# Performance work log

Measured on AMD Instinct MI355X. Metric: run time of the kernel, lower is better.

Reference implementation:

```python
import jax, jax.numpy as jnp
import numpy as np

N_GO, N_KE, D = 8000, 2000, 16
N_LAYERS, N_TISSUE, DRUG = 3, 512, 2048
B = 256


def _scatter_add(msgs, dst, n):
    # msgs: [B, E, D] -> [B, n, D], summing messages into destination nodes
    Bm, _, d = msgs.shape
    return jnp.zeros((Bm, n, d), msgs.dtype).at[:, dst, :].add(msgs)


def setup_inputs() -> dict:
    key = jax.random.key(0)
    ks = jax.random.split(key, 20)
    inp = {
        "x": jax.random.normal(ks[0], (B, N_GO + DRUG), jnp.float32),
        "go_ke_src": jax.random.randint(ks[1], (50000,), 0, N_GO),
        "go_ke_dst": jax.random.randint(ks[2], (50000,), 0, N_KE),
        "ke_ke_src": jax.random.randint(ks[3], (20000,), 0, N_KE),
        "ke_ke_dst": jax.random.randint(ks[4], (20000,), 0, N_KE),
        "tissue": jax.random.randint(ks[5], (N_TISSUE,), 0, N_KE),
    }
    def w(k, shape, fan_in):
        return jax.random.normal(k, shape, jnp.float32) / np.sqrt(fan_in)
    inp["W_dec"] = w(ks[6], (N_GO, D), 1.0)          # per-GO scalar->vector layer
    inp["b_dec"] = jnp.zeros((N_GO, D), jnp.float32)
    inp["W_g2k"] = w(ks[7], (D, D), D)
    inp["b_g2k"] = jnp.zeros((D,), jnp.float32)
    inp["W_kk"] = w(ks[8], (N_LAYERS, D, D), D)
    inp["b_kk"] = jnp.zeros((N_LAYERS, D), jnp.float32)
    inp["w_ke"] = w(ks[9], (D,), D)                   # node readout D->1
    inp["b_ke"] = jnp.zeros((), jnp.float32)
    inp["W_bio1"] = w(ks[10], (N_TISSUE, 256), N_TISSUE)
    inp["b_bio1"] = jnp.zeros((256,), jnp.float32)
    inp["W_bio2"] = w(ks[11], (256, 128), 256)
    inp["b_bio2"] = jnp.zeros((128,), jnp.float32)
    inp["W_drug1"] = w(ks[12], (DRUG, 512), DRUG)
    inp["b_drug1"] = jnp.zeros((512,), jnp.float32)
    inp["W_drug2"] = w(ks[13], (512, 128), 512)
    inp["b_drug2"] = jnp.zeros((128,), jnp.float32)
    inp["W_pred"] = w(ks[14], (256, 1), 256)
    inp["b_pred"] = jnp.zeros((1,), jnp.float32)
    return inp


def reference(x, go_ke_src, go_ke_dst, ke_ke_src, ke_ke_dst, tissue,
              W_dec, b_dec, W_g2k, b_g2k, W_kk, b_kk, w_ke, b_ke,
              W_bio1, b_bio1, W_bio2, b_bio2,
              W_drug1, b_drug1, W_drug2, b_drug2, W_pred, b_pred):
    # go_decode_layer: per-GO scalar -> D-dim node feature
    go = jnp.tanh(x[:, :-DRUG, None] * W_dec + b_dec)          # [B, N_GO, D]
    # go2ke: gather source GO features, scatter-add into KE nodes, transform
    ke = _scatter_add(go[:, go_ke_src, :], go_ke_dst, N_KE)    # [B, N_KE, D]
    ke = jnp.tanh(ke @ W_g2k + b_g2k)
    # ke2ke message-passing layers
    for l in range(W_kk.shape[0]):
        agg = _scatter_add(ke[:, ke_ke_src, :], ke_ke_dst, N_KE)
        ke = jnp.tanh((ke + agg) @ W_kk[l] + b_kk[l])
    # ke_layer: per-node readout D -> scalar
    ke = jnp.tanh(jnp.einsum('bnd,d->bn', ke, w_ke) + b_ke)    # [B, N_KE]
    # tissue gather + bio MLP head
    bio = ke[:, tissue]                                         # [B, N_TISSUE]
    bio = jax.nn.relu(bio @ W_bio1 + b_bio1)
    bio = jax.nn.relu(bio @ W_bio2 + b_bio2)
    # drug fingerprint MLP head
    drug = x[:, -DRUG:]
    drug = jax.nn.relu(drug @ W_drug1 + b_drug1)
    drug = jax.nn.relu(drug @ W_drug2 + b_drug2)
    # predictor on concatenated features
    comb = jnp.concatenate([bio, drug], axis=-1)                # [B, 256]
    return comb @ W_pred + b_pred                               # [B, 1]
```

## Files before the change

### kernel.cpp

```cpp
#include <hip/hip_runtime.h>
#include <hip/hip_bf16.h>
#include <cstdint>
#include <cstddef>

#define BATCH 256
#define NGO   8000
#define NKE   2000
#define DD    16
#define XCOLS 10048
#define NDRUG 2048
#define NT    512
#define NSLAB 8
#define SB    32

__device__ __forceinline__ float tanh_fast(float z) {
    float e = __builtin_amdgcn_exp2f(z * 2.885390081777926f);
    float r = __builtin_amdgcn_rcpf(e + 1.0f);
    return fmaf(-2.0f, r, 1.0f);
}

__device__ __forceinline__ void add4(float4& a, const float4 b) {
    a.x += b.x; a.y += b.y; a.z += b.z; a.w += b.w;
}

__global__ void k_hist2(const int* __restrict__ gd, const int* __restrict__ kd,
                        int* __restrict__ cg, int* __restrict__ ck, int Eg, int Ek) {
    int e = blockIdx.x * 256 + threadIdx.x;
    if (e < Eg) atomicAdd(&cg[gd[e]], 1);
    else if (e < Eg + Ek) atomicAdd(&ck[kd[e - Eg]], 1);
}

__global__ void k_scan2(const int* __restrict__ cnt_go, const int* __restrict__ cnt_kk,
                        int* __restrict__ rp_go, int* __restrict__ rp_kk) {
    const int* cnt = blockIdx.x ? cnt_kk : cnt_go;
    int* rowptr    = blockIdx.x ? rp_kk  : rp_go;
    __shared__ int s[2048];
    int t = threadIdx.x;
    s[t]        = (t        < NKE) ? cnt[t]        : 0;
    s[t + 1024] = (t + 1024 < NKE) ? cnt[t + 1024] : 0;
    __syncthreads();
    for (int st = 1; st < 2048; st <<= 1) {
        int v0 = (t >= st) ? s[t - st] : 0;
        int v1 = s[t + 1024 - st];
        __syncthreads();
        s[t] += v0; s[t + 1024] += v1;
        __syncthreads();
    }
    if (t == 0) rowptr[0] = 0;
    rowptr[t + 1] = s[t];
    if (t + 1024 < NKE) rowptr[t + 1025] = s[t + 1024];
}

__global__ void k_fill2(const int* __restrict__ gs, const int* __restrict__ gdst,
                        const int* __restrict__ ks, const int* __restrict__ kdst,
                        int Eg, int Ek,
                        const int* __restrict__ rp_go, int* __restrict__ cur_go, int* __restrict__ col_go,
                        const int* __restrict__ rp_kk, int* __restrict__ cur_kk, int* __restrict__ col_kk) {
    int e = blockIdx.x * 256 + threadIdx.x;
    if (e < Eg) {
        int d = gdst[e];
        int p = atomicAdd(&cur_go[d], 1);
        col_go[rp_go[d] + p] = gs[e];
    } else if (e < Eg + Ek) {
        int e2 = e - Eg;
        int d = kdst[e2];
        int p = atomicAdd(&cur_kk[d], 1);
        col_kk[rp_kk[d] + p] = ks[e2];
    }
}

__global__ __launch_bounds__(256) void k_txpose(const float* __restrict__ x, float* __restrict__ xT) {
    __shared__ float tile[64][69];
    int c4 = threadIdx.x & 15, rr = threadIdx.x >> 4;
    int n0 = blockIdx.x * 64, b0 = blockIdx.y * 64;
#pragma unroll
    for (int i = 0; i < 4; i++) {
        int row = rr + i * 16;
        float4 v = *(const float4*)&x[(size_t)(b0 + row) * XCOLS + n0 + c4 * 4];
        tile[row][c4 * 4 + 0] = v.x; tile[row][c4 * 4 + 1] = v.y;
        tile[row][c4 * 4 + 2] = v.z; tile[row][c4 * 4 + 3] = v.w;
    }
    __syncthreads();
#pragma unroll
    for (int i = 0; i < 4; i++) {
        int nrow = rr + i * 16;
        float4 w;
        w.x = tile[c4 * 4 + 0][nrow]; w.y = tile[c4 * 4 + 1][nrow];
        w.z = tile[c4 * 4 + 2][nrow]; w.w = tile[c4 * 4 + 3][nrow];
        *(float4*)&xT[(size_t)(n0 + nrow) * 256 + b0 + c4 * 4] = w;
    }
}

__global__ __launch_bounds__(128) void k_fuse(const float* __restrict__ xT,
                                              const int* __restrict__ rowptr,
                                              const int* __restrict__ col,
                                              const float* __restrict__ Wd,
                                              const float* __restrict__ bd,
                                              const float* __restrict__ W,
                                              const float* __restrict__ bias,
                                              float* __restrict__ ke) {
    __shared__ float pre[32 * 17];
    __shared__ float Ws[256];
    __shared__ float bs[16];
    int s = blockIdx.x & 7, n = blockIdx.x >> 3;
    int tid = threadIdx.x;
    Ws[tid] = W[tid]; Ws[tid + 128] = W[tid + 128];
    if (tid < 16) bs[tid] = bias[tid];
    int bloc = tid >> 2, d4 = tid & 3;
    int bglob = s * SB + bloc;
    const float4* Wd4 = (const float4*)Wd;
    const float4* bd4 = (const float4*)bd;

    float4 acc = make_float4(0, 0, 0, 0);
    int e = rowptr[n], end = rowptr[n + 1];
    for (; e + 1 < end; e += 2) {
        int s0 = col[e], s1 = col[e + 1];
        float  xv0 = xT[(size_t)s0 * 256 + bglob];
        float  xv1 = xT[(size_t)s1 * 256 + bglob];
        float4 w0 = Wd4[s0 * 4 + d4], w1 = Wd4[s1 * 4 + d4];
        float4 c0 = bd4[s0 * 4 + d4], c1 = bd4[s1 * 4 + d4];
        acc.x += tanh_fast(fmaf(xv0, w0.x, c0.x)) + tanh_fast(fmaf(xv1, w1.x, c1.x));
        acc.y += tanh_fast(fmaf(xv0, w0.y, c0.y)) + tanh_fast(fmaf(xv1, w1.y, c1.y));
        acc.z += tanh_fast(fmaf(xv0, w0.z, c0.z)) + tanh_fast(fmaf(xv1, w1.z, c1.z));
        acc.w += tanh_fast(fmaf(xv0, w0.w, c0.w)) + tanh_fast(fmaf(xv1, w1.w, c1.w));
    }
    if (e < end) {
        int s0 = col[e];
        float  xv0 = xT[(size_t)s0 * 256 + bglob];
        float4 w0 = Wd4[s0 * 4 + d4];
        float4 c0 = bd4[s0 * 4 + d4];
        acc.x += tanh_fast(fmaf(xv0, w0.x, c0.x));
        acc.y += tanh_fast(fmaf(xv0, w0.y, c0.y));
        acc.z += tanh_fast(fmaf(xv0, w0.z, c0.z));
        acc.w += tanh_fast(fmaf(xv0, w0.w, c0.w));
    }
    pre[bloc * 17 + d4 * 4 + 0] = acc.x;
    pre[bloc * 17 + d4 * 4 + 1] = acc.y;
    pre[bloc * 17 + d4 * 4 + 2] = acc.z;
    pre[bloc * 17 + d4 * 4 + 3] = acc.w;
    __syncthreads();

    float4 o;
    float* op = &o.x;
#pragma unroll
    for (int q = 0; q < 4; q++) {
        int dp = d4 * 4 + q;
        float a = bs[dp];
#pragma unroll
        for (int d = 0; d < 16; d++) a = fmaf(pre[bloc * 17 + d], Ws[d * 16 + dp], a);
        op[q] = tanh_fast(a);
    }
    *(float4*)&ke[((size_t)s * NKE + n) * 512 + bloc * 16 + d4 * 4] = o;
}

__global__ __launch_bounds__(128) void k_layer(const float* __restrict__ kin,
                                               const int* __restrict__ rowptr,
                                               const int* __restrict__ col,
                                               const float* __restrict__ W,
                                               const float* __restrict__ bias,
                                               float* __restrict__ kout) {
    __shared__ float pre[32 * 17];
    __shared__ float Ws[256];
    __shared__ float bs[16];
    int s = blockIdx.x & 7, n = blockIdx.x >> 3;
    int tid = threadIdx.x;
    Ws[tid] = W[tid]; Ws[tid + 128] = W[tid + 128];
    if (tid < 16) bs[tid] = bias[tid];
    int bloc = tid >> 2, d4 = tid & 3;
    size_t slab_base = (size_t)s * NKE * 512;

    float4 acc = *(const float4*)&kin[slab_base + (size_t)n * 512 + tid * 4];
    int e = rowptr[n], end = rowptr[n + 1];
    for (; e + 1 < end; e += 2) {
        float4 v0 = *(const float4*)&kin[slab_base + (size_t)col[e]     * 512 + tid * 4];
        float4 v1 = *(const float4*)&kin[slab_base + (size_t)col[e + 1] * 512 + tid * 4];
        add4(acc, v0); add4(acc, v1);
    }
    if (e < end) {
        float4 v0 = *(const float4*)&kin[slab_base + (size_t)col[e] * 512 + tid * 4];
        add4(acc, v0);
    }
    pre[bloc * 17 + d4 * 4 + 0] = acc.x;
    pre[bloc * 17 + d4 * 4 + 1] = acc.y;
    pre[bloc * 17 + d4 * 4 + 2] = acc.z;
    pre[bloc * 17 + d4 * 4 + 3] = acc.w;
    __syncthreads();

    float4 o;
    float* op = &o.x;
#pragma unroll
    for (int q = 0; q < 4; q++) {
        int dp = d4 * 4 + q;
        float a = bs[dp];
#pragma unroll
        for (int d = 0; d < 16; d++) a = fmaf(pre[bloc * 17 + d], Ws[d * 16 + dp], a);
        op[q] = tanh_fast(a);
    }
    *(float4*)&kout[slab_base + (size_t)n * 512 + bloc * 16 + d4 * 4] = o;
}

__global__ __launch_bounds__(256) void k_kescalar(const float* __restrict__ ke,
                                                  const int* __restrict__ tissue,
                                                  const float* __restrict__ wke,
                                                  const float* __restrict__ bke,
                                                  float* __restrict__ bioT) {
    int t = blockIdx.x, b = threadIdx.x;
    int n = tissue[t];
    int s = b >> 5, bloc = b & 31;
    const float4* kp = (const float4*)&ke[((size_t)s * NKE + n) * 512 + bloc * 16];
    const float4* wp = (const float4*)wke;
    float4 k0 = kp[0], k1 = kp[1], k2 = kp[2], k3 = kp[3];
    float4 w0 = wp[0], w1 = wp[1], w2 = wp[2], w3 = wp[3];
    float acc = bke[0];
    acc += k0.x * w0.x + k0.y * w0.y + k0.z * w0.z + k0.w * w0.w;
    acc += k1.x * w1.x + k1.y * w1.y + k1.z * w1.z + k1.w * w1.w;
    acc += k2.x * w2.x + k2.y * w2.y + k2.z * w2.z + k2.w * w2.w;
    acc += k3.x * w3.x + k3.y * w3.y + k3.z * w3.z + k3.w * w3.w;
    bioT[t * 256 + b] = tanh_fast(acc);
}

__global__ __launch_bounds__(256) void k_txd(const float* __restrict__ x, float* __restrict__ xdT) {
    int t = blockIdx.x, b = threadIdx.x;
    xdT[t * 256 + b] = x[(size_t)b * XCOLS + NGO + t];
}

__global__ __launch_bounds__(256) void k_gemm(const float* __restrict__ A,
                                              const float* __restrict__ W,
                                              float* __restrict__ Cpart,
                                              int N, int Kper) {
    __shared__ float As[32][68];
    __shared__ float Ws[32][68];
    int tid = threadIdx.x;
    int tx = tid & 15, ty = tid >> 4;
    int jt = blockIdx.x * 64, bt = blockIdx.y * 64;
    int ks = blockIdx.z;
    int k0 = ks * Kper;

    float acc[4][4];
#pragma unroll
    for (int i = 0; i < 4; i++)
#pragma unroll
        for (int j = 0; j < 4; j++) acc[i][j] = 0.0f;

    for (int kc = 0; kc < Kper; kc += 32) {
#pragma unroll
        for (int i = 0; i < 8; i++) {
            int idx = tid + i * 256;
            int kk = idx >> 6, cc = idx & 63;
            As[kk][cc] = A[(size_t)(k0 + kc + kk) * 256 + bt + cc];
            Ws[kk][cc] = W[(size_t)(k0 + kc + kk) * N + jt + cc];
        }
        __syncthreads();
#pragma unroll 8
        for (int kk = 0; kk < 32; kk++) {
            float4 a = *(const float4*)&As[kk][tx * 4];
            float4 w = *(const float4*)&Ws[kk][ty * 4];
            acc[0][0] = fmaf(w.x, a.x, acc[0][0]); acc[0][1] = fmaf(w.x, a.y, acc[0][1]);
            acc[0][2] = fmaf(w.x, a.z, acc[0][2]); acc[0][3] = fmaf(w.x, a.w, acc[0][3]);
            acc[1][0] = fmaf(w.y, a.x, acc[1][0]); acc[1][1] = fmaf(w.y, a.y, acc[1][1]);
            acc[1][2] = fmaf(w.y, a.z, acc[1][2]); acc[1][3] = fmaf(w.y, a.w, acc[1][3]);
            acc[2][0] = fmaf(w.z, a.x, acc[2][0]); acc[2][1] = fmaf(w.z, a.y, acc[2][1]);
            acc[2][2] = fmaf(w.z, a.z, acc[2][2]); acc[2][3] = fmaf(w.z, a.w, acc[2][3]);
            acc[3][0] = fmaf(w.w, a.x, acc[3][0]); acc[3][1] = fmaf(w.w, a.y, acc[3][1]);
            acc[3][2] = fmaf(w.w, a.z, acc[3][2]); acc[3][3] = fmaf(w.w, a.w, acc[3][3]);
        }
        __syncthreads();
    }
#pragma unroll
    for (int jy = 0; jy < 4; jy++) {
        int j = jt + ty * 4 + jy;
        float4 v = make_float4(acc[jy][0], acc[jy][1], acc[jy][2], acc[jy][3]);
        *(float4*)&Cpart[((size_t)ks * N + j) * 256 + bt + tx * 4] = v;
    }
}

__global__ __launch_bounds__(256) void k_red(const float* __restrict__ Cpart,
                                             const float* __restrict__ bias,
                                             float* __restrict__ C, int N, int S) {
    int j = blockIdx.x, b = threadIdx.x;
    float acc = bias[j];
    for (int s = 0; s < S; s++) acc += Cpart[((size_t)s * N + j) * 256 + b];
    C[j * 256 + b] = fmaxf(acc, 0.0f);
}

__global__ __launch_bounds__(256) void k_final(const float* __restrict__ bio2T,
                                               const float* __restrict__ drug2T,
                                               const float* __restrict__ Wp,
                                               const float* __restrict__ bp,
                                               float* __restrict__ out) {
    int b = threadIdx.x;
    float acc = bp[0];
#pragma unroll 8
    for (int i = 0; i < 128; i++) acc = fmaf(bio2T[i * 256 + b], Wp[i], acc);
#pragma unroll 8
    for (int i = 0; i < 128; i++) acc = fmaf(drug2T[i * 256 + b], Wp[128 + i], acc);
    out[b] = acc;
}

extern "C" void kernel_launch(void* const* d_in, const int* in_sizes, int n_in,
                              void* d_out, int out_size, void* d_ws, size_t ws_size,
                              hipStream_t stream) {
    const float* x       = (const float*)d_in[0];
    const int*   go_src  = (const int*)d_in[1];
    const int*   go_dst  = (const int*)d_in[2];
    const int*   kk_src  = (const int*)d_in[3];
    const int*   kk_dst  = (const int*)d_in[4];
    const int*   tissue  = (const int*)d_in[5];
    const float* W_dec   = (const float*)d_in[6];
    const float* b_dec   = (const float*)d_in[7];
    const float* W_g2k   = (const float*)d_in[8];
    const float* b_g2k   = (const float*)d_in[9];
    const float* W_kk    = (const float*)d_in[10];
    const float* b_kk    = (const float*)d_in[11];
    const float* w_ke    = (const float*)d_in[12];
    const float* b_ke    = (const float*)d_in[13];
    const float* W_bio1  = (const float*)d_in[14];
    const float* b_bio1  = (const float*)d_in[15];
    const float* W_bio2  = (const float*)d_in[16];
    const float* b_bio2  = (const float*)d_in[17];
    const float* W_drug1 = (const float*)d_in[18];
    const float* b_drug1 = (const float*)d_in[19];
    const float* W_drug2 = (const float*)d_in[20];
    const float* b_drug2 = (const float*)d_in[21];
    const float* W_pred  = (const float*)d_in[22];
    const float* b_pred  = (const float*)d_in[23];
    float* out = (float*)d_out;

    const int E_GO = in_sizes[1];
    const int E_KK = in_sizes[3];

    char* wsb = (char*)d_ws;
    size_t off = 0;
    float* xT      = (float*)(wsb + off); off += (size_t)NGO * 256 * 4;
    float* ke_a    = (float*)(wsb + off); off += (size_t)NSLAB * NKE * 512 * 4;
    float* ke_b    = (float*)(wsb + off); off += (size_t)NSLAB * NKE * 512 * 4;
    float* bio_inT = (float*)(wsb + off); off += (size_t)NT * 256 * 4;
    float* bio1T   = (float*)(wsb + off); off += (size_t)256 * 256 * 4;
    float* bio2T   = (float*)(wsb + off); off += (size_t)128 * 256 * 4;
    float* xdT     = (float*)(wsb + off); off += (size_t)NDRUG * 256 * 4;
    float* drug1T  = (float*)(wsb + off); off += (size_t)512 * 256 * 4;
    float* drug2T  = (float*)(wsb + off); off += (size_t)128 * 256 * 4;
    float* cpart   = (float*)(wsb + off); off += (size_t)8 * 512 * 256 * 4;
    int* cnt_go    = (int*)(wsb + off); off += 2048 * 4;
    int* cur_go    = (int*)(wsb + off); off += 2048 * 4;
    int* cnt_kk    = (int*)(wsb + off); off += 2048 * 4;
    int* cur_kk    = (int*)(wsb + off); off += 2048 * 4;
    int* rp_go     = (int*)(wsb + off); off += 2048 * 4;
    int* rp_kk     = (int*)(wsb + off); off += 2048 * 4;
    int* col_go    = (int*)(wsb + off); off += 50048 * 4;
    int* col_kk    = (int*)(wsb + off); off += 20048 * 4;

    hipMemsetAsync(cnt_go, 0, 4 * 2048 * 4, stream);

    int Etot = E_GO + E_KK;
    k_hist2<<<(Etot + 255) / 256, 256, 0, stream>>>(go_dst, kk_dst, cnt_go, cnt_kk, E_GO, E_KK);
    k_scan2<<<2, 1024, 0, stream>>>(cnt_go, cnt_kk, rp_go, rp_kk);
    k_fill2<<<(Etot + 255) / 256, 256, 0, stream>>>(go_src, go_dst, kk_src, kk_dst, E_GO, E_KK,
                                                    rp_go, cur_go, col_go, rp_kk, cur_kk, col_kk);

    k_txpose<<<dim3(NGO / 64, 4), 256, 0, stream>>>(x, xT);
    k_fuse<<<NKE * NSLAB, 128, 0, stream>>>(xT, rp_go, col_go, W_dec, b_dec, W_g2k, b_g2k, ke_a);
    k_layer<<<NKE * NSLAB, 128, 0, stream>>>(ke_a, rp_kk, col_kk, W_kk + 0 * 256, b_kk + 0 * 16, ke_b);
    k_layer<<<NKE * NSLAB, 128, 0, stream>>>(ke_b, rp_kk, col_kk, W_kk + 1 * 256, b_kk + 1 * 16, ke_a);
    k_layer<<<NKE * NSLAB, 128, 0, stream>>>(ke_a, rp_kk, col_kk, W_kk + 2 * 256, b_kk + 2 * 16, ke_b);
    k_kescalar<<<NT, 256, 0, stream>>>(ke_b, tissue, w_ke, b_ke, bio_inT);

    k_txd<<<NDRUG, 256, 0, stream>>>(x, xdT);
    k_gemm<<<dim3(512 / 64, 4, 8), 256, 0, stream>>>(xdT, W_drug1, cpart, 512, 2048 / 8);
    k_red<<<512, 256, 0, stream>>>(cpart, b_drug1, drug1T, 512, 8);
    k_gemm<<<dim3(128 / 64, 4, 4), 256, 0, stream>>>(drug1T, W_drug2, cpart, 128, 512 / 4);
    k_red<<<128, 256, 0, stream>>>(cpart, b_drug2, drug2T, 128, 4);

    k_gemm<<<dim3(256 / 64, 4, 4), 256, 0, stream>>>(bio_inT, W_bio1, cpart, 256, 512 / 4);
    k_red<<<256, 256, 0, stream>>>(cpart, b_bio1, bio1T, 256, 4);
    k_gemm<<<dim3(128 / 64, 4, 2), 256, 0, stream>>>(bio1T, W_bio2, cpart, 128, 256 / 2);
    k_red<<<128, 256, 0, stream>>>(cpart, b_bio2, bio2T, 128, 2);

    k_final<<<1, 256, 0, stream>>>(bio2T, drug2T, W_pred, b_pred, out);
}
```

Measured before the change: 244.2 us.

## Fuse split-K reductions into consumers, merge transposes, prescale tanh inputs

Merges the GO transpose, drug transpose and a bias prescale into one prep kernel. The split-K reduce kernels are removed: each consumer GEMM or the final kernel now sums the partials and applies bias and ReLU while loading. In the fused gather kernel the inputs and biases are prescaled by the tanh constant, and the -2 and +1 tanh terms are hoisted out of the edge loop using the node degree. The k_layer gather loop is unrolled from 2 to 4 loads. Together these cut launch count and per-edge arithmetic, at the cost of redundant partial-sum reads inside the GEMM tile loads.

```diff
diff --git a/kernel.cpp b/kernel.cpp
--- a/kernel.cpp
+++ b/kernel.cpp
@@ -12,11 +12,17 @@
 #define NT    512
 #define NSLAB 8
 #define SB    32
+#define TANH_SCALE 2.885390081777926f
 
 __device__ __forceinline__ float tanh_fast(float z) {
-    float e = __builtin_amdgcn_exp2f(z * 2.885390081777926f);
+    float e = __builtin_amdgcn_exp2f(z * TANH_SCALE);
     float r = __builtin_amdgcn_rcpf(e + 1.0f);
     return fmaf(-2.0f, r, 1.0f);
+}
+
+__device__ __forceinline__ float rcp_core(float zp) {
+    float e = __builtin_amdgcn_exp2f(zp);
+    return __builtin_amdgcn_rcpf(e + 1.0f);
 }
 
 __device__ __forceinline__ void add4(float4& a, const float4 b) {
@@ -69,10 +75,23 @@
     }
 }
 
-__global__ __launch_bounds__(256) void k_txpose(const float* __restrict__ x, float* __restrict__ xT) {
+__global__ __launch_bounds__(256) void k_prep(const float* __restrict__ x,
+                                              float* __restrict__ xT,
+                                              float* __restrict__ xdT,
+                                              const float* __restrict__ bd,
+                                              float* __restrict__ bds) {
+    int bid = blockIdx.x;
+    if (bid >= 628) {
+        int i = (bid - 628) * 256 + threadIdx.x;
+        bds[i] = bd[i] * TANH_SCALE;
+        return;
+    }
     __shared__ float tile[64][69];
     int c4 = threadIdx.x & 15, rr = threadIdx.x >> 4;
-    int n0 = blockIdx.x * 64, b0 = blockIdx.y * 64;
+    int n0, b0;
+    bool isgo = bid < 500;
+    if (isgo) { n0 = (bid % 125) * 64; b0 = (bid / 125) * 64; }
+    else      { int t = bid - 500; n0 = NGO + (t & 31) * 64; b0 = (t >> 5) * 64; }
 #pragma unroll
     for (int i = 0; i < 4; i++) {
         int row = rr + i * 16;
@@ -87,7 +106,12 @@
         float4 w;
         w.x = tile[c4 * 4 + 0][nrow]; w.y = tile[c4 * 4 + 1][nrow];
         w.z = tile[c4 * 4 + 2][nrow]; w.w = tile[c4 * 4 + 3][nrow];
-        *(float4*)&xT[(size_t)(n0 + nrow) * 256 + b0 + c4 * 4] = w;
+        if (isgo) {
+            w.x *= TANH_SCALE; w.y *= TANH_SCALE; w.z *= TANH_SCALE; w.w *= TANH_SCALE;
+            *(float4*)&xT[(size_t)(n0 + nrow) * 256 + b0 + c4 * 4] = w;
+        } else {
+            *(float4*)&xdT[(size_t)(n0 - NGO + nrow) * 256 + b0 + c4 * 4] = w;
+        }
     }
 }
 
@@ -95,7 +119,7 @@
                                               const int* __restrict__ rowptr,
                                               const int* __restrict__ col,
                                               const float* __restrict__ Wd,
-                                              const float* __restrict__ bd,
+                                              const float* __restrict__ bds,
                                               const float* __restrict__ W,
                                               const float* __restrict__ bias,
                                               float* __restrict__ ke) {
@@ -109,35 +133,36 @@
     int bloc = tid >> 2, d4 = tid & 3;
     int bglob = s * SB + bloc;
     const float4* Wd4 = (const float4*)Wd;
-    const float4* bd4 = (const float4*)bd;
-
+    const float4* bd4 = (const float4*)bds;
+
+    int e = rowptr[n], end = rowptr[n + 1];
+    float degF = (float)(end - e);
     float4 acc = make_float4(0, 0, 0, 0);
-    int e = rowptr[n], end = rowptr[n + 1];
     for (; e + 1 < end; e += 2) {
         int s0 = col[e], s1 = col[e + 1];
         float  xv0 = xT[(size_t)s0 * 256 + bglob];
         float  xv1 = xT[(size_t)s1 * 256 + bglob];
         float4 w0 = Wd4[s0 * 4 + d4], w1 = Wd4[s1 * 4 + d4];
         float4 c0 = bd4[s0 * 4 + d4], c1 = bd4[s1 * 4 + d4];
-        acc.x += tanh_fast(fmaf(xv0, w0.x, c0.x)) + tanh_fast(fmaf(xv1, w1.x, c1.x));
-        acc.y += tanh_fast(fmaf(xv0, w0.y, c0.y)) + tanh_fast(fmaf(xv1, w1.y, c1.y));
-        acc.z += tanh_fast(fmaf(xv0, w0.z, c0.z)) + tanh_fast(fmaf(xv1, w1.z, c1.z));
-        acc.w += tanh_fast(fmaf(xv0, w0.w, c0.w)) + tanh_fast(fmaf(xv1, w1.w, c1.w));
+        acc.x += rcp_core(fmaf(xv0, w0.x, c0.x)) + rcp_core(fmaf(xv1, w1.x, c1.x));
+        acc.y += rcp_core(fmaf(xv0, w0.y, c0.y)) + rcp_core(fmaf(xv1, w1.y, c1.y));
+        acc.z += rcp_core(fmaf(xv0, w0.z, c0.z)) + rcp_core(fmaf(xv1, w1.z, c1.z));
+        acc.w += rcp_core(fmaf(xv0, w0.w, c0.w)) + rcp_core(fmaf(xv1, w1.w, c1.w));
     }
     if (e < end) {
         int s0 = col[e];
         float  xv0 = xT[(size_t)s0 * 256 + bglob];
         float4 w0 = Wd4[s0 * 4 + d4];
         float4 c0 = bd4[s0 * 4 + d4];
-        acc.x += tanh_fast(fmaf(xv0, w0.x, c0.x));
-        acc.y += tanh_fast(fmaf(xv0, w0.y, c0.y));
-        acc.z += tanh_fast(fmaf(xv0, w0.z, c0.z));
-        acc.w += tanh_fast(fmaf(xv0, w0.w, c0.w));
-    }
-    pre[bloc * 17 + d4 * 4 + 0] = acc.x;
-    pre[bloc * 17 + d4 * 4 + 1] = acc.y;
-    pre[bloc * 17 + d4 * 4 + 2] = acc.z;
-    pre[bloc * 17 + d4 * 4 + 3] = acc.w;
+        acc.x += rcp_core(fmaf(xv0, w0.x, c0.x));
+        acc.y += rcp_core(fmaf(xv0, w0.y, c0.y));
+        acc.z += rcp_core(fmaf(xv0, w0.z, c0.z));
+        acc.w += rcp_core(fmaf(xv0, w0.w, c0.w));
+    }
+    pre[bloc * 17 + d4 * 4 + 0] = fmaf(-2.0f, acc.x, degF);
+    pre[bloc * 17 + d4 * 4 + 1] = fmaf(-2.0f, acc.y, degF);
+    pre[bloc * 17 + d4 * 4 + 2] = fmaf(-2.0f, acc.z, degF);
+    pre[bloc * 17 + d4 * 4 + 3] = fmaf(-2.0f, acc.w, degF);
     __syncthreads();
 
     float4 o;
@@ -171,12 +196,14 @@
 
     float4 acc = *(const float4*)&kin[slab_base + (size_t)n * 512 + tid * 4];
     int e = rowptr[n], end = rowptr[n + 1];
-    for (; e + 1 < end; e += 2) {
+    for (; e + 3 < end; e += 4) {
         float4 v0 = *(const float4*)&kin[slab_base + (size_t)col[e]     * 512 + tid * 4];
         float4 v1 = *(const float4*)&kin[slab_base + (size_t)col[e + 1] * 512 + tid * 4];
-        add4(acc, v0); add4(acc, v1);
-    }
-    if (e < end) {
+        float4 v2 = *(const float4*)&kin[slab_base + (size_t)col[e + 2] * 512 + tid * 4];
+        float4 v3 = *(const float4*)&kin[slab_base + (size_t)col[e + 3] * 512 + tid * 4];
+        add4(acc, v0); add4(acc, v1); add4(acc, v2); add4(acc, v3);
+    }
+    for (; e < end; ++e) {
         float4 v0 = *(const float4*)&kin[slab_base + (size_t)col[e] * 512 + tid * 4];
         add4(acc, v0);
     }
@@ -219,15 +246,11 @@
     bioT[t * 256 + b] = tanh_fast(acc);
 }
 
-__global__ __launch_bounds__(256) void k_txd(const float* __restrict__ x, float* __restrict__ xdT) {
-    int t = blockIdx.x, b = threadIdx.x;
-    xdT[t * 256 + b] = x[(size_t)b * XCOLS + NGO + t];
-}
-
-__global__ __launch_bounds__(256) void k_gemm(const float* __restrict__ A,
+__global__ __launch_bounds__(256) void k_gemm(const float* __restrict__ Asrc,
                                               const float* __restrict__ W,
+                                              const float* __restrict__ bprev,
                                               float* __restrict__ Cpart,
-                                              int N, int Kper) {
+                                              int N, int Kper, int Kdim, int Sprev) {
     __shared__ float As[32][68];
     __shared__ float Ws[32][68];
     int tid = threadIdx.x;
@@ -247,8 +270,18 @@
         for (int i = 0; i < 8; i++) {
             int idx = tid + i * 256;
             int kk = idx >> 6, cc = idx & 63;
-            As[kk][cc] = A[(size_t)(k0 + kc + kk) * 256 + bt + cc];
-            Ws[kk][cc] = W[(size_t)(k0 + kc + kk) * N + jt + cc];
+            int kg = k0 + kc + kk;
+            float a;
+            if (Sprev == 0) {
+                a = Asrc[(size_t)kg * 256 + bt + cc];
+            } else {
+                a = bprev[kg];
+                for (int s = 0; s < Sprev; s++)
+                    a += Asrc[((size_t)s * Kdim + kg) * 256 + bt + cc];
+                a = fmaxf(a, 0.0f);
+            }
+            As[kk][cc] = a;
+            Ws[kk][cc] = W[(size_t)kg * N + jt + cc];
         }
         __syncthreads();
 #pragma unroll 8
@@ -274,26 +307,31 @@
     }
 }
 
-__global__ __launch_bounds__(256) void k_red(const float* __restrict__ Cpart,
-                                             const float* __restrict__ bias,
-                                             float* __restrict__ C, int N, int S) {
-    int j = blockIdx.x, b = threadIdx.x;
-    float acc = bias[j];
-    for (int s = 0; s < S; s++) acc += Cpart[((size_t)s * N + j) * 256 + b];
-    C[j * 256 + b] = fmaxf(acc, 0.0f);
-}
-
-__global__ __launch_bounds__(256) void k_final(const float* __restrict__ bio2T,
-                                               const float* __restrict__ drug2T,
+__global__ __launch_bounds__(256) void k_final(const float* __restrict__ cpd2,
+                                               const float* __restrict__ cpb2,
+                                               const float* __restrict__ b_d2,
+                                               const float* __restrict__ b_b2,
                                                const float* __restrict__ Wp,
                                                const float* __restrict__ bp,
                                                float* __restrict__ out) {
     int b = threadIdx.x;
     float acc = bp[0];
-#pragma unroll 8
-    for (int i = 0; i < 128; i++) acc = fmaf(bio2T[i * 256 + b], Wp[i], acc);
-#pragma unroll 8
-    for (int i = 0; i < 128; i++) acc = fmaf(drug2T[i * 256 + b], Wp[128 + i], acc);
+#pragma unroll 4
+    for (int i = 0; i < 128; i++) {
+        float v = b_b2[i];
+        v += cpb2[((size_t)0 * 128 + i) * 256 + b];
+        v += cpb2[((size_t)1 * 128 + i) * 256 + b];
+        acc = fmaf(fmaxf(v, 0.0f), Wp[i], acc);
+    }
+#pragma unroll 4
+    for (int i = 0; i < 128; i++) {
+        float v = b_d2[i];
+        v += cpd2[((size_t)0 * 128 + i) * 256 + b];
+        v += cpd2[((size_t)1 * 128 + i) * 256 + b];
+        v += cpd2[((size_t)2 * 128 + i) * 256 + b];
+        v += cpd2[((size_t)3 * 128 + i) * 256 + b];
+        acc = fmaf(fmaxf(v, 0.0f), Wp[128 + i], acc);
+    }
     out[b] = acc;
 }
 
@@ -335,12 +373,12 @@
     float* ke_a    = (float*)(wsb + off); off += (size_t)NSLAB * NKE * 512 * 4;
     float* ke_b    = (float*)(wsb + off); off += (size_t)NSLAB * NKE * 512 * 4;
     float* bio_inT = (float*)(wsb + off); off += (size_t)NT * 256 * 4;
-    float* bio1T   = (float*)(wsb + off); off += (size_t)256 * 256 * 4;
-    float* bio2T   = (float*)(wsb + off); off += (size_t)128 * 256 * 4;
     float* xdT     = (float*)(wsb + off); off += (size_t)NDRUG * 256 * 4;
-    float* drug1T  = (float*)(wsb + off); off += (size_t)512 * 256 * 4;
-    float* drug2T  = (float*)(wsb + off); off += (size_t)128 * 256 * 4;
-    float* cpart   = (float*)(wsb + off); off += (size_t)8 * 512 * 256 * 4;
+    float* bds     = (float*)(wsb + off); off += (size_t)NGO * 16 * 4;
+    float* cp_d1   = (float*)(wsb + off); off += (size_t)8 * 512 * 256 * 4;
+    float* cp_d2   = (float*)(wsb + off); off += (size_t)4 * 128 * 256 * 4;
+    float* cp_b1   = (float*)(wsb + off); off += (size_t)4 * 256 * 256 * 4;
+    float* cp_b2   = (float*)(wsb + off); off += (size_t)2 * 128 * 256 * 4;
     int* cnt_go    = (int*)(wsb + off); off += 2048 * 4;
     int* cur_go    = (int*)(wsb + off); off += 2048 * 4;
     int* cnt_kk    = (int*)(wsb + off); off += 2048 * 4;
@@ -358,23 +396,19 @@
     k_fill2<<<(Etot + 255) / 256, 256, 0, stream>>>(go_src, go_dst, kk_src, kk_dst, E_GO, E_KK,
                                                     rp_go, cur_go, col_go, rp_kk, cur_kk, col_kk);
 
-    k_txpose<<<dim3(NGO / 64, 4), 256, 0, stream>>>(x, xT);
-    k_fuse<<<NKE * NSLAB, 128, 0, stream>>>(xT, rp_go, col_go, W_dec, b_dec, W_g2k, b_g2k, ke_a);
+    k_prep<<<1128, 256, 0, stream>>>(x, xT, xdT, b_dec, bds);
+
+    k_fuse<<<NKE * NSLAB, 128, 0, stream>>>(xT, rp_go, col_go, W_dec, bds, W_g2k, b_g2k, ke_a);
     k_layer<<<NKE * NSLAB, 128, 0, stream>>>(ke_a, rp_kk, col_kk, W_kk + 0 * 256, b_kk + 0 * 16, ke_b);
     k_layer<<<NKE * NSLAB, 128, 0, stream>>>(ke_b, rp_kk, col_kk, W_kk + 1 * 256, b_kk + 1 * 16, ke_a);
     k_layer<<<NKE * NSLAB, 128, 0, stream>>>(ke_a, rp_kk, col_kk, W_kk + 2 * 256, b_kk + 2 * 16, ke_b);
     k_kescalar<<<NT, 256, 0, stream>>>(ke_b, tissue, w_ke, b_ke, bio_inT);
 
-    k_txd<<<NDRUG, 256, 0, stream>>>(x, xdT);
-    k_gemm<<<dim3(512 / 64, 4, 8), 256, 0, stream>>>(xdT, W_drug1, cpart, 512, 2048 / 8);
-    k_red<<<512, 256, 0, stream>>>(cpart, b_drug1, drug1T, 512, 8);
-    k_gemm<<<dim3(128 / 64, 4, 4), 256, 0, stream>>>(drug1T, W_drug2, cpart, 128, 512 / 4);
-    k_red<<<128, 256, 0, stream>>>(cpart, b_drug2, drug2T, 128, 4);
-
-    k_gemm<<<dim3(256 / 64, 4, 4), 256, 0, stream>>>(bio_inT, W_bio1, cpart, 256, 512 / 4);
-    k_red<<<256, 256, 0, stream>>>(cpart, b_bio1, bio1T, 256, 4);
-    k_gemm<<<dim3(128 / 64, 4, 2), 256, 0, stream>>>(bio1T, W_bio2, cpart, 128, 256 / 2);
-    k_red<<<128, 256, 0, stream>>>(cpart, b_bio2, bio2T, 128, 2);
-
-    k_final<<<1, 256, 0, stream>>>(bio2T, drug2T, W_pred, b_pred, out);
-}
+    k_gemm<<<dim3(8, 4, 8), 256, 0, stream>>>(xdT, W_drug1, nullptr, cp_d1, 512, 256, 0, 0);
+    k_gemm<<<dim3(2, 4, 4), 256, 0, stream>>>(cp_d1, W_drug2, b_drug1, cp_d2, 128, 128, 512, 8);
+
+    k_gemm<<<dim3(4, 4, 4), 256, 0, stream>>>(bio_inT, W_bio1, nullptr, cp_b1, 256, 128, 0, 0);
+    k_gemm<<<dim3(2, 4, 2), 256, 0, stream>>>(cp_b1, W_bio2, b_bio1, cp_b2, 128, 128, 256, 4);
+
+    k_final<<<1, 256, 0, stream>>>(cp_d2, cp_b2, b_drug2, b_bio2, W_pred, b_pred, out);
+}
```

Result: slower. 361.6 us (+48.1%).
